# Kernel optimization log

Hardware: AMD Instinct MI355X
Metric: run time of the kernel (lower is better)

The kernel has to match this reference:

```python
import jax, jax.numpy as jnp
import numpy as np

B, L, K, NR, S = 512, 1024, 8, 512, 20  # batch, seq_len, n_matrices, n_rates, alphabet
EXT = 26  # extended alphabet (20 std aa + 6 special), pad of 6 in call()


def _expm(A):
    """Differentiable matrix exponential for small batched matrices (..., n, n).
    Scaling-and-squaring with an order-16 Taylor series (fixed 6 squarings).
    Matches tf.linalg.expm to high accuracy for the small-norm tau*Q here."""
    SQ = 6
    A = A / jnp.asarray(2.0 ** SQ, A.dtype)
    n = A.shape[-1]
    I = jnp.eye(n, dtype=A.dtype)
    P = I + A
    T = A
    for i in range(2, 17):
        T = jnp.matmul(T, A) / i
        P = P + T
    for _ in range(SQ):
        P = jnp.matmul(P, P)
    return P


def setup_inputs() -> dict:
    key = jax.random.key(0)
    k1, k2, k3, k4, k5 = jax.random.split(key, 5)
    return {
        "inputs": jax.random.randint(k1, (B, L), 0, EXT, dtype=jnp.int32),
        "rate_indices": jax.random.randint(k2, (B,), 0, NR, dtype=jnp.int32),
        "tau_kernel": jax.random.normal(k3, (NR,), dtype=jnp.float32),
        "exchangeability_kernel": jax.random.normal(k4, (K, S, S), dtype=jnp.float32),
        "frequencies": jax.random.uniform(k5, (S,), dtype=jnp.float32, minval=0.01, maxval=1.0),
    }


def reference(inputs, rate_indices, tau_kernel, exchangeability_kernel, frequencies):
    b, l = inputs.shape
    mask = inputs < S                                   # (b, L) std-aa mask
    std = jnp.where(mask, inputs, 0)                    # clamp special tokens to 0
    maskf = mask.astype(jnp.float32)[:, :, None, None]  # (b, L, 1, 1)

    # make_R: symmetrize, softplus, zero diagonal
    eye = jnp.eye(S, dtype=jnp.float32)
    R = jax.nn.softplus(0.5 * (exchangeability_kernel + jnp.swapaxes(exchangeability_kernel, -1, -2)))
    R = R * (1.0 - eye)

    # make_rate_matrix: Q = R * pi, subtract row-sum diagonal, normalize by expected rate
    Q = R * frequencies[None, None, :]                  # (k, s, s)
    diag = jnp.sum(Q, axis=-1, keepdims=True)           # (k, s, 1)
    Q = Q - diag * eye
    mue = jnp.sum(frequencies[None, :, None] * diag, axis=-2, keepdims=True)  # (k, 1, 1)
    Q = Q / jnp.maximum(mue, 1e-16)

    # per-sequence evolutionary times
    tau = jax.nn.softplus(tau_kernel)[rate_indices]     # (b,)

    # batched small-matrix expm: (b, k, s, s)
    P = _expm(tau[:, None, None, None] * Q[None])

    # gather ancestral probability rows: (b, L, k, s)
    anc = P[jnp.arange(b)[:, None], :, std, :]
    anc = anc * maskf
    anc = jnp.pad(anc, ((0, 0), (0, 0), (0, 0), (0, EXT - S)))  # pad 20 -> 26
    rest = jax.nn.one_hot(inputs, EXT, dtype=jnp.float32)[:, :, None, :] * (1.0 - maskf)
    anc = anc + rest                                    # (b, L, k, 26)
    return anc.reshape(b, l, -1)                        # (b, L, k*26)
```

## Files before the change

### kernel.cpp

```cpp
#include <hip/hip_runtime.h>
#include <math.h>

#define B   512
#define L   1024
#define K   8
#define NR  512
#define S   20
#define EXT 26
#define SS  (S*S)
#define PD  24
#define ROWF (K*EXT)
#define BROW (L*ROWF)
#define HROW (BROW/2)

__device__ __forceinline__ float softplusf(float x) {
    return fmaxf(x, 0.0f) + log1pf(expf(-fabsf(x)));
}

__global__ __launch_bounds__(64, 4) void expm_kernel(
    const float* __restrict__ exch,
    const float* __restrict__ freq,
    const float* __restrict__ tau_kernel,
    const int*   __restrict__ rate_indices,
    float* __restrict__ out)
{
    int blk = blockIdx.x;
    int b = blk / K, kk = blk % K;

    __shared__ __align__(16) float M0[PD*PD];
    __shared__ __align__(16) float M1[PD*PD];
    __shared__ float diag_sh[S];
    __shared__ float mue_sh, tau_sh;

    int t = threadIdx.x;
    int li = t >> 3, lj = t & 7;
    int r0 = 3*li, c0 = 3*lj;

    for (int e = t; e < PD*PD; e += 64) { M0[e] = 0.f; M1[e] = 0.f; }
    if (t == 0) tau_sh = softplusf(tau_kernel[rate_indices[b]]);
    __syncthreads();

    const float* E = exch + kk * SS;
    for (int e = t; e < SS; e += 64) {
        int r = e / S, c = e - r*S;
        float v = 0.f;
        if (r != c)
            v = softplusf(0.5f * (E[r*S + c] + E[c*S + r])) * freq[c];
        M0[r*PD + c] = v;
    }
    __syncthreads();
    if (t < S) {
        float d = 0.f;
        #pragma unroll
        for (int j = 0; j < S; ++j) d += M0[t*PD + j];
        diag_sh[t] = d;
    }
    __syncthreads();
    if (t == 0) {
        float m = 0.f;
        #pragma unroll
        for (int s = 0; s < S; ++s) m += freq[s] * diag_sh[s];
        mue_sh = fmaxf(m, 1e-16f);
    }
    __syncthreads();

    float scale = tau_sh * 0.015625f;
    for (int e = t; e < SS; e += 64) {
        int r = e / S, c = e - r*S;
        float v = (r == c) ? -diag_sh[r] : M0[r*PD + c];
        M0[r*PD + c] = (v / mue_sh) * scale;
    }
    __syncthreads();

    float Ac[S][3];
    #pragma unroll
    for (int j = 0; j < S; ++j) {
        #pragma unroll
        for (int d = 0; d < 3; ++d)
            Ac[j][d] = M0[j*PD + c0 + d];
    }

    float P[3][3];
    #pragma unroll
    for (int dr = 0; dr < 3; ++dr)
        #pragma unroll
        for (int dc = 0; dc < 3; ++dc) {
            int r = r0 + dr, c = c0 + dc;
            P[dr][dc] = M0[r*PD + c] + ((r == c && r < S) ? 1.f : 0.f);
        }

    const float* Tc = M0;
    float* Tn = M1;
    #pragma unroll 1
    for (int i = 2; i <= 16; ++i) {
        float C[3][3] = {{0.f,0.f,0.f},{0.f,0.f,0.f},{0.f,0.f,0.f}};
        #pragma unroll
        for (int jc = 0; jc < 5; ++jc) {
            float4 a0 = *(const float4*)&Tc[(r0+0)*PD + 4*jc];
            float4 a1 = *(const float4*)&Tc[(r0+1)*PD + 4*jc];
            float4 a2 = *(const float4*)&Tc[(r0+2)*PD + 4*jc];
            float t0[4] = {a0.x, a0.y, a0.z, a0.w};
            float t1[4] = {a1.x, a1.y, a1.z, a1.w};
            float t2[4] = {a2.x, a2.y, a2.z, a2.w};
            #pragma unroll
            for (int dj = 0; dj < 4; ++dj) {
                int j = 4*jc + dj;
                #pragma unroll
                for (int dc = 0; dc < 3; ++dc) {
                    C[0][dc] = fmaf(t0[dj], Ac[j][dc], C[0][dc]);
                    C[1][dc] = fmaf(t1[dj], Ac[j][dc], C[1][dc]);
                    C[2][dc] = fmaf(t2[dj], Ac[j][dc], C[2][dc]);
                }
            }
        }
        float inv = 1.0f / (float)i;
        #pragma unroll
        for (int dr = 0; dr < 3; ++dr)
            #pragma unroll
            for (int dc = 0; dc < 3; ++dc) {
                C[dr][dc] *= inv;
                P[dr][dc] += C[dr][dc];
                Tn[(r0+dr)*PD + c0 + dc] = C[dr][dc];
            }
        __syncthreads();
        float* tmp = (float*)Tc; Tc = Tn; Tn = tmp;
    }

    #pragma unroll 1
    for (int sq = 0; sq < 6; ++sq) {
        #pragma unroll
        for (int dr = 0; dr < 3; ++dr)
            #pragma unroll
            for (int dc = 0; dc < 3; ++dc)
                Tn[(r0+dr)*PD + c0 + dc] = P[dr][dc];
        __syncthreads();
        const float* Pb = Tn;
        float C[3][3] = {{0.f,0.f,0.f},{0.f,0.f,0.f},{0.f,0.f,0.f}};
        #pragma unroll
        for (int jc = 0; jc < 5; ++jc) {
            float4 a0 = *(const float4*)&Pb[(r0+0)*PD + 4*jc];
            float4 a1 = *(const float4*)&Pb[(r0+1)*PD + 4*jc];
            float4 a2 = *(const float4*)&Pb[(r0+2)*PD + 4*jc];
            float t0[4] = {a0.x, a0.y, a0.z, a0.w};
            float t1[4] = {a1.x, a1.y, a1.z, a1.w};
            float t2[4] = {a2.x, a2.y, a2.z, a2.w};
            float cb[4][3];
            #pragma unroll
            for (int dj = 0; dj < 4; ++dj)
                #pragma unroll
                for (int dc = 0; dc < 3; ++dc)
                    cb[dj][dc] = Pb[(4*jc + dj)*PD + c0 + dc];
            #pragma unroll
            for (int dj = 0; dj < 4; ++dj)
                #pragma unroll
                for (int dc = 0; dc < 3; ++dc) {
                    C[0][dc] = fmaf(t0[dj], cb[dj][dc], C[0][dc]);
                    C[1][dc] = fmaf(t1[dj], cb[dj][dc], C[1][dc]);
                    C[2][dc] = fmaf(t2[dj], cb[dj][dc], C[2][dc]);
                }
        }
        #pragma unroll
        for (int dr = 0; dr < 3; ++dr)
            #pragma unroll
            for (int dc = 0; dc < 3; ++dc)
                P[dr][dc] = C[dr][dc];
        float* tmp = (float*)Tc; Tc = Tn; Tn = tmp;
    }

    size_t obase = (size_t)b * BROW + (size_t)kk * SS;
    #pragma unroll
    for (int dr = 0; dr < 3; ++dr) {
        int r = r0 + dr; if (r >= S) continue;
        #pragma unroll
        for (int dc = 0; dc < 3; ++dc) {
            int c = c0 + dc; if (c >= S) continue;
            float v = P[dr][dc];
            out[obase + r*S + c] = v;
            out[obase + HROW + r*S + c] = v;
        }
    }
}

__global__ __launch_bounds__(512, 8) void write_kernel(
    const int* __restrict__ inputs,
    float* __restrict__ out)
{
    __shared__ __align__(16) float Psh[K*SS];
    __shared__ __align__(16) float Row[EXT*ROWF];
    __shared__ int inp_sh[512];

    int blk = blockIdx.x;
    int b = blk >> 1, h = blk & 1;
    int t = threadIdx.x;

    float* base = out + (size_t)b * BROW + (size_t)h * HROW;

    const float4* src4 = (const float4*)base;
    float4* Psh4 = (float4*)Psh;
    for (int u = t; u < (K*SS)/4; u += 512) Psh4[u] = src4[u];
    inp_sh[t] = inputs[b * L + h * (L/2) + t];
    __syncthreads();

    for (int u = t; u < EXT*ROWF; u += 512) {
        int row = u / ROWF;
        int c   = u - row * ROWF;
        int k   = c / EXT;
        int s   = c - k * EXT;
        float v;
        if (row < S) v = (s < S) ? Psh[k*SS + row*S + s] : 0.f;
        else         v = (s == row) ? 1.f : 0.f;
        Row[u] = v;
    }
    __syncthreads();

    float4* out4 = (float4*)base;
    for (int u = t; u < (L/2) * (ROWF/4); u += 512) {
        int l = u / (ROWF/4);
        int q = u - l * (ROWF/4);
        const float4* r4 = (const float4*)(Row + inp_sh[l] * ROWF);
        out4[u] = r4[q];
    }
}

extern "C" void kernel_launch(void* const* d_in, const int* in_sizes, int n_in,
                              void* d_out, int out_size, void* d_ws, size_t ws_size,
                              hipStream_t stream) {
    const int*   inputs  = (const int*)  d_in[0];
    const int*   rate_ix = (const int*)  d_in[1];
    const float* tau_k   = (const float*)d_in[2];
    const float* exch    = (const float*)d_in[3];
    const float* freq    = (const float*)d_in[4];
    float* out = (float*)d_out;

    (void)d_ws; (void)ws_size;

    expm_kernel<<<B * K, 64, 0, stream>>>(exch, freq, tau_k, rate_ix, out);
    write_kernel<<<B * 2, 512, 0, stream>>>(inputs, out);
}
```

Baseline: 504.2 us.

## Fuse expm and row-broadcast write into one kernel per batch

Merges the two kernels so each 512-thread block handles one batch element, with its 8 waves each computing one matrix exponential into shared memory. The block then writes the gathered output rows directly. This removes the round trip of P through the output buffer in global memory and the second launch. In exchange, the grid has only 512 blocks, there is more shared memory per block and more block-wide barriers, and the memory-bound write phase cannot begin until each block's expm finishes, which may reduce occupancy and overlap.

After: 493.9 us. -2.0%, faster.

```diff
diff --git a/kernel.cpp b/kernel.cpp
--- a/kernel.cpp
+++ b/kernel.cpp
@@ -1,47 +1,62 @@
 #include <hip/hip_runtime.h>
 #include <math.h>
 
-#define B   512
-#define L   1024
-#define K   8
-#define NR  512
-#define S   20
-#define EXT 26
-#define SS  (S*S)
-#define PD  24
+#define B    512
+#define L    1024
+#define K    8
+#define NR   512
+#define S    20
+#define EXT  26
+#define SS   (S*S)
+#define PD   24
+#define PDSQ (PD*PD)
 #define ROWF (K*EXT)
 #define BROW (L*ROWF)
-#define HROW (BROW/2)
 
 __device__ __forceinline__ float softplusf(float x) {
     return fmaxf(x, 0.0f) + log1pf(expf(-fabsf(x)));
 }
 
-__global__ __launch_bounds__(64, 4) void expm_kernel(
+__global__ __launch_bounds__(512, 2) void fused_kernel(
+    const int*   __restrict__ inputs,
+    const int*   __restrict__ rate_indices,
+    const float* __restrict__ tau_kernel,
     const float* __restrict__ exch,
     const float* __restrict__ freq,
-    const float* __restrict__ tau_kernel,
-    const int*   __restrict__ rate_indices,
     float* __restrict__ out)
 {
-    int blk = blockIdx.x;
-    int b = blk / K, kk = blk % K;
-
-    __shared__ __align__(16) float M0[PD*PD];
-    __shared__ __align__(16) float M1[PD*PD];
-    __shared__ float diag_sh[S];
-    __shared__ float mue_sh, tau_sh;
-
-    int t = threadIdx.x;
-    int li = t >> 3, lj = t & 7;
-    int r0 = 3*li, c0 = 3*lj;
-
-    for (int e = t; e < PD*PD; e += 64) { M0[e] = 0.f; M1[e] = 0.f; }
+    __shared__ __align__(16) float M[K][2][PDSQ];
+    __shared__ __align__(16) float Row[EXT*ROWF];
+    __shared__ int   inp_sh[L];
+    __shared__ float diag_sh[K][S];
+    __shared__ float mue_sh[K];
+    __shared__ float tau_sh;
+
+    const int b    = blockIdx.x;
+    const int t    = threadIdx.x;
+    const int w    = t >> 6;
+    const int lane = t & 63;
+    const int li = lane >> 3, lj = lane & 7;
+    const int r0 = 3*li, c0 = 3*lj;
+
+    for (int u = t; u < L; u += 512) inp_sh[u] = inputs[b*L + u];
+    for (int e = t; e < EXT*ROWF; e += 512) {
+        int row = e / ROWF, c = e - row*ROWF;
+        int k = c / EXT, s = c - k*EXT;
+        Row[e] = (row >= S && s == row) ? 1.f : 0.f;
+    }
+    {
+        float* Mw = &M[w][0][0];
+        for (int e = lane; e < 2*PDSQ; e += 64) Mw[e] = 0.f;
+    }
     if (t == 0) tau_sh = softplusf(tau_kernel[rate_indices[b]]);
     __syncthreads();
 
-    const float* E = exch + kk * SS;
-    for (int e = t; e < SS; e += 64) {
+    float* M0 = &M[w][0][0];
+    float* M1 = &M[w][1][0];
+    const float* E = exch + w * SS;
+
+    for (int e = lane; e < SS; e += 64) {
         int r = e / S, c = e - r*S;
         float v = 0.f;
         if (r != c)
@@ -49,26 +64,28 @@
         M0[r*PD + c] = v;
     }
     __syncthreads();
-    if (t < S) {
+    if (lane < S) {
         float d = 0.f;
         #pragma unroll
-        for (int j = 0; j < S; ++j) d += M0[t*PD + j];
-        diag_sh[t] = d;
-    }
-    __syncthreads();
-    if (t == 0) {
+        for (int j = 0; j < S; ++j) d += M0[lane*PD + j];
+        diag_sh[w][lane] = d;
+    }
+    __syncthreads();
+    if (lane == 0) {
         float m = 0.f;
         #pragma unroll
-        for (int s = 0; s < S; ++s) m += freq[s] * diag_sh[s];
-        mue_sh = fmaxf(m, 1e-16f);
-    }
-    __syncthreads();
-
-    float scale = tau_sh * 0.015625f;
-    for (int e = t; e < SS; e += 64) {
-        int r = e / S, c = e - r*S;
-        float v = (r == c) ? -diag_sh[r] : M0[r*PD + c];
-        M0[r*PD + c] = (v / mue_sh) * scale;
+        for (int s = 0; s < S; ++s) m += freq[s] * diag_sh[w][s];
+        mue_sh[w] = fmaxf(m, 1e-16f);
+    }
+    __syncthreads();
+    {
+        float scale = tau_sh * 0.015625f;
+        float mue   = mue_sh[w];
+        for (int e = lane; e < SS; e += 64) {
+            int r = e / S, c = e - r*S;
+            float v = (r == c) ? -diag_sh[w][r] : M0[r*PD + c];
+            M0[r*PD + c] = (v / mue) * scale;
+        }
     }
     __syncthreads();
 
@@ -165,60 +182,26 @@
             for (int dc = 0; dc < 3; ++dc)
                 P[dr][dc] = C[dr][dc];
         float* tmp = (float*)Tc; Tc = Tn; Tn = tmp;
-    }
-
-    size_t obase = (size_t)b * BROW + (size_t)kk * SS;
+        __syncthreads();
+    }
+
     #pragma unroll
     for (int dr = 0; dr < 3; ++dr) {
         int r = r0 + dr; if (r >= S) continue;
         #pragma unroll
         for (int dc = 0; dc < 3; ++dc) {
             int c = c0 + dc; if (c >= S) continue;
-            float v = P[dr][dc];
-            out[obase + r*S + c] = v;
-            out[obase + HROW + r*S + c] = v;
-        }
-    }
-}
-
-__global__ __launch_bounds__(512, 8) void write_kernel(
-    const int* __restrict__ inputs,
-    float* __restrict__ out)
-{
-    __shared__ __align__(16) float Psh[K*SS];
-    __shared__ __align__(16) float Row[EXT*ROWF];
-    __shared__ int inp_sh[512];
-
-    int blk = blockIdx.x;
-    int b = blk >> 1, h = blk & 1;
-    int t = threadIdx.x;
-
-    float* base = out + (size_t)b * BROW + (size_t)h * HROW;
-
-    const float4* src4 = (const float4*)base;
-    float4* Psh4 = (float4*)Psh;
-    for (int u = t; u < (K*SS)/4; u += 512) Psh4[u] = src4[u];
-    inp_sh[t] = inputs[b * L + h * (L/2) + t];
-    __syncthreads();
-
-    for (int u = t; u < EXT*ROWF; u += 512) {
-        int row = u / ROWF;
-        int c   = u - row * ROWF;
-        int k   = c / EXT;
-        int s   = c - k * EXT;
-        float v;
-        if (row < S) v = (s < S) ? Psh[k*SS + row*S + s] : 0.f;
-        else         v = (s == row) ? 1.f : 0.f;
-        Row[u] = v;
-    }
-    __syncthreads();
-
-    float4* out4 = (float4*)base;
-    for (int u = t; u < (L/2) * (ROWF/4); u += 512) {
+            Row[r*ROWF + w*EXT + c] = P[dr][dc];
+        }
+    }
+    __syncthreads();
+
+    const float4* Row4 = (const float4*)Row;
+    float4* out4 = (float4*)out + (size_t)b * (BROW/4);
+    for (int u = t; u < L * (ROWF/4); u += 512) {
         int l = u / (ROWF/4);
         int q = u - l * (ROWF/4);
-        const float4* r4 = (const float4*)(Row + inp_sh[l] * ROWF);
-        out4[u] = r4[q];
+        out4[u] = Row4[inp_sh[l] * (ROWF/4) + q];
     }
 }
 
@@ -234,6 +217,5 @@
 
     (void)d_ws; (void)ws_size;
 
-    expm_kernel<<<B * K, 64, 0, stream>>>(exch, freq, tau_k, rate_ix, out);
-    write_kernel<<<B * 2, 512, 0, stream>>>(inputs, out);
+    fused_kernel<<<B, 512, 0, stream>>>(inputs, rate_ix, tau_k, exch, freq, out);
 }
```
